# Optimization experiments

Hardware: AMD Instinct MI355X
Metric: run time of the kernel (lower is better)

Reference implementation:

```python
import jax, jax.numpy as jnp
import numpy as np

# graph layout constants
B = 64        # number of graphs
NPG = 512     # nodes per graph
N = B * NPG   # total nodes
DEG = 16      # avg degree
E = N * DEG   # total edges
F_IN = 256
H, C = 4, 64  # heads, per-head dim
K = NPG // 2  # topk pooling keeps ratio=0.5 per graph


def setup_inputs() -> dict:
    key = jax.random.key(0)
    ks = jax.random.split(key, 8)
    x = jax.random.normal(ks[0], (N, F_IN), dtype=jnp.float32)
    # within-graph random edges (src -> dst), contiguous node ids per graph
    offs = jnp.repeat(jnp.arange(B, dtype=jnp.int64) * NPG, NPG * DEG)
    src = offs + jax.random.randint(ks[1], (E,), 0, NPG)
    dst = offs + jax.random.randint(ks[2], (E,), 0, NPG)
    edge_index = jnp.stack([src, dst]).astype(jnp.int64)
    W = jax.random.normal(ks[3], (F_IN, H, C), dtype=jnp.float32) / np.sqrt(F_IN)
    att_src = jax.random.normal(ks[4], (H, C), dtype=jnp.float32) / np.sqrt(C)
    att_dst = jax.random.normal(ks[5], (H, C), dtype=jnp.float32) / np.sqrt(C)
    bias = jnp.zeros((H * C,), dtype=jnp.float32)
    bn_gamma = jnp.ones((H * C,), dtype=jnp.float32)
    bn_beta = jnp.zeros((H * C,), dtype=jnp.float32)
    pool_weight = jax.random.normal(ks[6], (H * C,), dtype=jnp.float32) / np.sqrt(H * C)
    return {"x": x, "edge_index": edge_index, "W": W, "att_src": att_src,
            "att_dst": att_dst, "bias": bias, "bn_gamma": bn_gamma,
            "bn_beta": bn_beta, "pool_weight": pool_weight}


def reference(x, edge_index, W, att_src, att_dst, bias, bn_gamma, bn_beta, pool_weight):
    n = x.shape[0]
    # --- GATConv ---
    h = jnp.einsum('nf,fhc->nhc', x, W)                 # [N,H,C]
    a_src = jnp.sum(h * att_src, axis=-1)               # [N,H]
    a_dst = jnp.sum(h * att_dst, axis=-1)               # [N,H]
    loops = jnp.arange(n, dtype=edge_index.dtype)        # add_self_loops=True default
    src = jnp.concatenate([edge_index[0], loops])
    dst = jnp.concatenate([edge_index[1], loops])
    e = jax.nn.leaky_relu(a_src[src] + a_dst[dst], 0.2)  # [E+N,H]
    # scatter-softmax over edges grouped by destination node
    emax = jax.ops.segment_max(e, dst, num_segments=n)
    ex = jnp.exp(e - emax[dst])
    den = jax.ops.segment_sum(ex, dst, num_segments=n)
    alpha = ex / (den[dst] + 1e-16)                      # [E+N,H]
    msg = alpha[:, :, None] * h[src]                     # [E+N,H,C]
    out = jax.ops.segment_sum(msg, dst, num_segments=n)  # [N,H,C]
    feat = out.reshape(n, H * C) + bias                  # concat heads
    # --- ReLU + BatchNorm (batch stats, training mode) ---
    feat = jax.nn.relu(feat)
    mean = jnp.mean(feat, axis=0)
    var = jnp.var(feat, axis=0)
    feat = (feat - mean) * jax.lax.rsqrt(var + 1e-5) * bn_gamma + bn_beta
    # --- TopKPooling (score = x.w/||w||, keep top ratio per graph, gate by tanh) ---
    score = feat @ pool_weight / jnp.linalg.norm(pool_weight)  # [N]
    top_s, top_i = jax.lax.top_k(score.reshape(B, NPG), K)     # [B,K]
    fg = feat.reshape(B, NPG, H * C)
    sel = jnp.take_along_axis(fg, top_i[:, :, None], axis=1)    # [B,K,HC]
    pooled = sel * jnp.tanh(top_s)[:, :, None]
    return pooled.reshape(B * K, H * C)
```

## Files before the change

### kernel.cpp

```cpp
#include <hip/hip_runtime.h>
#include <math.h>

#define N_NODES 32768
#define NPG 512
#define NGRAPH 64
#define KKEEP 256
#define CAP 64

typedef __attribute__((ext_vector_type(8))) short short8;
typedef __attribute__((ext_vector_type(4))) float f32x4;

__device__ __forceinline__ unsigned short f2bf(float v) {
  unsigned u = __builtin_bit_cast(unsigned, v);
  u = (u + 0x7FFFu + ((u >> 16) & 1u)) >> 16;
  return (unsigned short)u;
}
__device__ __forceinline__ float bf2f(unsigned short u) {
  unsigned v = ((unsigned)u) << 16;
  return __builtin_bit_cast(float, v);
}

__global__ __launch_bounds__(256) void k_hist_conv(
    const int* __restrict__ ei, int E, int* __restrict__ cnt,
    unsigned short* __restrict__ nbr,
    const float* __restrict__ x, const float* __restrict__ W,
    unsigned short* __restrict__ xh, unsigned short* __restrict__ xl,
    unsigned short* __restrict__ wth, unsigned short* __restrict__ wtl,
    unsigned short* __restrict__ wtll) {
  const int t = threadIdx.x;
  if (blockIdx.x < 2048) {
    int e = blockIdx.x * 256 + t;
    if (e < E) {
      int s = ei[e];
      int d = ei[E + e];
      int slot = atomicAdd(&cnt[d], 1);
      if (slot < CAP) nbr[(size_t)d * CAP + slot] = (unsigned short)(s & (NPG - 1));
    }
  } else if (blockIdx.x < 4096) {
    size_t base = ((size_t)(blockIdx.x - 2048) * 256 + t) * 16;
    unsigned short hb[16], lb[16];
#pragma unroll
    for (int g = 0; g < 4; g++) {
      float4 v = *(const float4*)&x[base + g * 4];
      float f[4] = {v.x, v.y, v.z, v.w};
#pragma unroll
      for (int j = 0; j < 4; j++) {
        unsigned short hh = f2bf(f[j]);
        float e1 = f[j] - bf2f(hh);
        hb[g * 4 + j] = hh;
        lb[g * 4 + j] = f2bf(e1);
      }
    }
    *(uint4*)&xh[base] = *(uint4*)&hb[0];
    *(uint4*)&xh[base + 8] = *(uint4*)&hb[8];
    *(uint4*)&xl[base] = *(uint4*)&lb[0];
    *(uint4*)&xl[base + 8] = *(uint4*)&lb[8];
  } else {
    int bw = blockIdx.x - 4096;
    int n = bw * 4 + (t >> 6);
    int k = (t & 63) * 4;
    unsigned short hb[4], lb[4], qb[4];
#pragma unroll
    for (int j = 0; j < 4; j++) {
      float v = W[(size_t)(k + j) * 256 + n];
      unsigned short hh = f2bf(v);
      float e1 = v - bf2f(hh);
      unsigned short ll = f2bf(e1);
      float e2 = e1 - bf2f(ll);
      hb[j] = hh; lb[j] = ll; qb[j] = f2bf(e2);
    }
    *(uint2*)&wth[(size_t)n * 256 + k] = *(uint2*)&hb[0];
    *(uint2*)&wtl[(size_t)n * 256 + k] = *(uint2*)&lb[0];
    *(uint2*)&wtll[(size_t)n * 256 + k] = *(uint2*)&qb[0];
  }
}

__global__ __launch_bounds__(256) void k_gemm(
    const float* __restrict__ x,
    const unsigned short* __restrict__ xhp, const unsigned short* __restrict__ xlp,
    const unsigned short* __restrict__ wth, const unsigned short* __restrict__ wtl,
    const unsigned short* __restrict__ wtll,
    const float* __restrict__ attS, const float* __restrict__ attD,
    float* __restrict__ h, float* __restrict__ a_src, float* __restrict__ a_dst) {
  __shared__ unsigned short As[3][128][40];
  __shared__ unsigned short Bs[3][128][40];
  const int t = threadIdx.x;
  const int mb = blockIdx.x >> 1, nh = blockIdx.x & 1;
  const int row0 = mb * 128;
  const int wid = t >> 6, lane = t & 63;
  const int q = lane >> 4, ln = lane & 15;
  const int wm = (wid >> 1) * 64, wn = (wid & 1) * 64;
  f32x4 acc[4][4] = {};

  for (int kc = 0; kc < 8; kc++) {
    const int k0 = kc * 32;
#pragma unroll
    for (int i = 0; i < 2; i++) {
      int c = i * 256 + t;
      int r = c >> 2, ko = (c & 3) * 8;
      size_t ga = (size_t)(row0 + r) * 256 + k0 + ko;
      uint4 vh = *(const uint4*)&xhp[ga];
      uint4 vl = *(const uint4*)&xlp[ga];
      *(uint4*)&As[0][r][ko] = vh;
      *(uint4*)&As[1][r][ko] = vl;
      float4 f0 = *(const float4*)&x[ga];
      float4 f1 = *(const float4*)&x[ga + 4];
      unsigned short hs[8], ls[8], qs[8];
      *(uint4*)&hs[0] = vh;
      *(uint4*)&ls[0] = vl;
      float ff[8] = {f0.x, f0.y, f0.z, f0.w, f1.x, f1.y, f1.z, f1.w};
#pragma unroll
      for (int j = 0; j < 8; j++)
        qs[j] = f2bf(ff[j] - bf2f(hs[j]) - bf2f(ls[j]));
      *(uint4*)&As[2][r][ko] = *(uint4*)&qs[0];
      size_t gb = (size_t)(nh * 128 + r) * 256 + k0 + ko;
      *(uint4*)&Bs[0][r][ko] = *(const uint4*)&wth[gb];
      *(uint4*)&Bs[1][r][ko] = *(const uint4*)&wtl[gb];
      *(uint4*)&Bs[2][r][ko] = *(const uint4*)&wtll[gb];
    }
    __syncthreads();
    short8 ah[4], al[4], aq[4];
#pragma unroll
    for (int mt = 0; mt < 4; mt++) {
      ah[mt] = *(const short8*)&As[0][wm + mt * 16 + ln][q * 8];
      al[mt] = *(const short8*)&As[1][wm + mt * 16 + ln][q * 8];
      aq[mt] = *(const short8*)&As[2][wm + mt * 16 + ln][q * 8];
    }
#pragma unroll
    for (int nt = 0; nt < 4; nt++) {
      short8 bh = *(const short8*)&Bs[0][wn + nt * 16 + ln][q * 8];
      short8 bl = *(const short8*)&Bs[1][wn + nt * 16 + ln][q * 8];
      short8 bq = *(const short8*)&Bs[2][wn + nt * 16 + ln][q * 8];
#pragma unroll
      for (int mt = 0; mt < 4; mt++) {
        acc[mt][nt] = __builtin_amdgcn_mfma_f32_16x16x32_bf16(ah[mt], bh, acc[mt][nt], 0, 0, 0);
        acc[mt][nt] = __builtin_amdgcn_mfma_f32_16x16x32_bf16(ah[mt], bl, acc[mt][nt], 0, 0, 0);
        acc[mt][nt] = __builtin_amdgcn_mfma_f32_16x16x32_bf16(al[mt], bh, acc[mt][nt], 0, 0, 0);
        acc[mt][nt] = __builtin_amdgcn_mfma_f32_16x16x32_bf16(ah[mt], bq, acc[mt][nt], 0, 0, 0);
        acc[mt][nt] = __builtin_amdgcn_mfma_f32_16x16x32_bf16(al[mt], bl, acc[mt][nt], 0, 0, 0);
        acc[mt][nt] = __builtin_amdgcn_mfma_f32_16x16x32_bf16(aq[mt], bh, acc[mt][nt], 0, 0, 0);
      }
    }
    __syncthreads();
  }
  const int head = nh * 2 + (wid & 1);
  float sA[4], sD[4];
#pragma unroll
  for (int nt = 0; nt < 4; nt++) {
    int n = nh * 128 + wn + nt * 16 + ln;
    sA[nt] = attS[n];
    sD[nt] = attD[n];
  }
#pragma unroll
  for (int mt = 0; mt < 4; mt++) {
#pragma unroll
    for (int reg = 0; reg < 4; reg++) {
      int m = row0 + wm + mt * 16 + q * 4 + reg;
      float ps = 0.f, pd = 0.f;
#pragma unroll
      for (int nt = 0; nt < 4; nt++) {
        float v = acc[mt][nt][reg];
        h[(size_t)m * 256 + nh * 128 + wn + nt * 16 + ln] = v;
        ps = fmaf(v, sA[nt], ps);
        pd = fmaf(v, sD[nt], pd);
      }
#pragma unroll
      for (int d = 1; d < 16; d <<= 1) {
        ps += __shfl_xor(ps, d, 16);
        pd += __shfl_xor(pd, d, 16);
      }
      if (ln == 0) {
        a_src[m * 4 + head] = ps;
        a_dst[m * 4 + head] = pd;
      }
    }
  }
}

__global__ __launch_bounds__(256) void k_agg(
    const float* __restrict__ h, const float* __restrict__ a_src,
    const float* __restrict__ a_dst, const int* __restrict__ cnt,
    const unsigned short* __restrict__ nbr, const float* __restrict__ bias,
    float* __restrict__ feat) {
  __shared__ float p_lds[4][68][4];
  __shared__ int s_lds[4][68];
  const int wv = threadIdx.x >> 6;
  const int lane = threadIdx.x & 63;
  int nb = (blockIdx.x & 7) * (N_NODES / 4 / 8) + (blockIdx.x >> 3);
  const int node = nb * 4 + wv;
  const int head = lane >> 4;
  const int li = lane & 15;
  const int c0 = lane * 4;
  const int base = node & ~(NPG - 1);
  const float ad = a_dst[node * 4 + head];
  int n = cnt[node];
  if (n > CAP) n = CAP;
  float e_reg[5];
  int srcs[5];
  int nit = 0;
  float m = -1e30f;
  for (int j = li; j <= n; j += 16) {
    int s = (j < n) ? base + (int)nbr[(size_t)node * CAP + j] : node;
    float e = a_src[s * 4 + head] + ad;
    e = (e > 0.f) ? e : 0.2f * e;
    srcs[nit] = s;
    e_reg[nit++] = e;
    m = fmaxf(m, e);
  }
#pragma unroll
  for (int d = 1; d < 16; d <<= 1) m = fmaxf(m, __shfl_xor(m, d, 16));
  float l = 0.f;
  for (int i = 0; i < nit; i++) {
    int j = li + i * 16;
    float p = __expf(e_reg[i] - m);
    l += p;
    p_lds[wv][j][head] = p;
    if (head == 0) s_lds[wv][j] = srcs[i];
  }
#pragma unroll
  for (int d = 1; d < 16; d <<= 1) l += __shfl_xor(l, d, 16);
  const float linv = 1.f / (l + 1e-16f);
  __builtin_amdgcn_s_waitcnt(0);
  float4 acc0 = make_float4(0.f, 0.f, 0.f, 0.f);
  float4 acc1 = make_float4(0.f, 0.f, 0.f, 0.f);
  int j = 0;
  for (; j + 1 <= n; j += 2) {
    float p0 = p_lds[wv][j][head];
    float p1 = p_lds[wv][j + 1][head];
    int s0 = s_lds[wv][j];
    int s1 = s_lds[wv][j + 1];
    float4 h0 = *(const float4*)&h[(size_t)s0 * 256 + c0];
    float4 h1 = *(const float4*)&h[(size_t)s1 * 256 + c0];
    acc0.x = fmaf(p0, h0.x, acc0.x); acc1.x = fmaf(p1, h1.x, acc1.x);
    acc0.y = fmaf(p0, h0.y, acc0.y); acc1.y = fmaf(p1, h1.y, acc1.y);
    acc0.z = fmaf(p0, h0.z, acc0.z); acc1.z = fmaf(p1, h1.z, acc1.z);
    acc0.w = fmaf(p0, h0.w, acc0.w); acc1.w = fmaf(p1, h1.w, acc1.w);
  }
  if (j <= n) {
    float p0 = p_lds[wv][j][head];
    int s0 = s_lds[wv][j];
    float4 h0 = *(const float4*)&h[(size_t)s0 * 256 + c0];
    acc0.x = fmaf(p0, h0.x, acc0.x);
    acc0.y = fmaf(p0, h0.y, acc0.y);
    acc0.z = fmaf(p0, h0.z, acc0.z);
    acc0.w = fmaf(p0, h0.w, acc0.w);
  }
  const float4 b4 = *(const float4*)&bias[c0];
  float4 o;
  o.x = fmaxf(fmaf(acc0.x + acc1.x, linv, b4.x), 0.f);
  o.y = fmaxf(fmaf(acc0.y + acc1.y, linv, b4.y), 0.f);
  o.z = fmaxf(fmaf(acc0.z + acc1.z, linv, b4.z), 0.f);
  o.w = fmaxf(fmaf(acc0.w + acc1.w, linv, b4.w), 0.f);
  *(float4*)&feat[(size_t)node * 256 + c0] = o;
}

__global__ __launch_bounds__(256) void k_bn_partial(const float* __restrict__ feat,
                                                    double* __restrict__ psum,
                                                    double* __restrict__ psq) {
  const int c = threadIdx.x;
  const int r0 = blockIdx.x * 128;
  double s = 0.0, q = 0.0;
  for (int i = 0; i < 128; i++) {
    double v = (double)feat[(size_t)(r0 + i) * 256 + c];
    s += v;
    q += v * v;
  }
  psum[blockIdx.x * 256 + c] = s;
  psq[blockIdx.x * 256 + c] = q;
}

__global__ __launch_bounds__(1024) void k_bn_final(
    const double* __restrict__ psum, const double* __restrict__ psq,
    const float* __restrict__ gam, const float* __restrict__ bet,
    const float* __restrict__ pw, float* __restrict__ cA, float* __restrict__ cB,
    float* __restrict__ sv) {
  __shared__ double reds[4][256];
  __shared__ double redq[4][256];
  __shared__ double wsq[256];
  __shared__ double sb[256];
  const int t = threadIdx.x;
  const int c = t & 255, sl = t >> 8;
  double s = 0.0, q = 0.0;
  for (int i = sl * 64; i < sl * 64 + 64; i++) {
    s += psum[i * 256 + c];
    q += psq[i * 256 + c];
  }
  reds[sl][c] = s;
  redq[sl][c] = q;
  if (sl == 0) {
    double w = (double)pw[c];
    wsq[c] = w * w;
  }
  __syncthreads();
  if (t == 0) {
    double nn = 0.0;
    for (int i = 0; i < 256; i++) nn += wsq[i];
    wsq[0] = sqrt(nn);
  }
  __syncthreads();
  if (sl == 0) {
    s = reds[0][c] + reds[1][c] + reds[2][c] + reds[3][c];
    q = redq[0][c] + redq[1][c] + redq[2][c] + redq[3][c];
    double mean = s / (double)N_NODES;
    double var = q / (double)N_NODES - mean * mean;
    double a = (double)gam[c] / sqrt(var + 1e-5);
    double cb = (double)bet[c] - mean * a;
    cA[c] = (float)a;
    cB[c] = (float)cb;
    double pwnv = (double)pw[c] / wsq[0];
    sv[c] = (float)(a * pwnv);
    sb[c] = cb * pwnv;
  }
  __syncthreads();
  if (t == 0) {
    double s0 = 0.0;
    for (int i = 0; i < 256; i++) s0 += sb[i];
    sv[256] = (float)s0;
  }
}

__global__ __launch_bounds__(256) void k_score(
    const float* __restrict__ feat, const float* __restrict__ sv,
    float* __restrict__ score) {
  const int lane = threadIdx.x & 63;
  const int node = blockIdx.x * 4 + (threadIdx.x >> 6);
  const int c0 = lane * 4;
  float4 f = *(const float4*)&feat[(size_t)node * 256 + c0];
  float4 w = *(const float4*)&sv[c0];
  float p = f.x * w.x + f.y * w.y + f.z * w.z + f.w * w.w;
#pragma unroll
  for (int d = 1; d < 64; d <<= 1) p += __shfl_xor(p, d, 64);
  if (lane == 0) score[node] = p + sv[256];
}

__global__ __launch_bounds__(256) void k_topk(
    const float* __restrict__ score, const float* __restrict__ feat,
    const float* __restrict__ cA, const float* __restrict__ cB,
    float* __restrict__ out) {
  __shared__ float ss[NPG];
  __shared__ int rnk[64];
  __shared__ float gt[64];
  const int g = blockIdx.x >> 3;
  const int part = blockIdx.x & 7;
  const int t = threadIdx.x;
  ss[t] = score[g * NPG + t];
  ss[t + 256] = score[g * NPG + t + 256];
  __syncthreads();
  const int ln = t & 3;
  const int ndl = part * 64 + (t >> 2);
  const float s = ss[ndl];
  int rank = 0;
  for (int j = ln * 128; j < ln * 128 + 128; j++) {
    float sj = ss[j];
    rank += (sj > s || (sj == s && j < ndl)) ? 1 : 0;
  }
  rank += __shfl_xor(rank, 1);
  rank += __shfl_xor(rank, 2);
  if (ln == 0) {
    rnk[t >> 2] = rank;
    gt[t >> 2] = tanhf(s);
  }
  __syncthreads();
  for (int idx = t; idx < 64 * 64; idx += 256) {
    int r = idx >> 6;
    int rank2 = rnk[r];
    if (rank2 < KKEEP) {
      int c4 = (idx & 63) * 4;
      int node = g * NPG + part * 64 + r;
      float4 f = *(const float4*)&feat[(size_t)node * 256 + c4];
      float4 a = *(const float4*)&cA[c4];
      float4 b = *(const float4*)&cB[c4];
      float tg = gt[r];
      float4 o;
      o.x = fmaf(f.x, a.x, b.x) * tg;
      o.y = fmaf(f.y, a.y, b.y) * tg;
      o.z = fmaf(f.z, a.z, b.z) * tg;
      o.w = fmaf(f.w, a.w, b.w) * tg;
      *(float4*)&out[(size_t)(g * KKEEP + rank2) * 256 + c4] = o;
    }
  }
}

extern "C" void kernel_launch(void* const* d_in, const int* in_sizes, int n_in,
                              void* d_out, int out_size, void* d_ws, size_t ws_size,
                              hipStream_t stream) {
  const float* x    = (const float*)d_in[0];
  const int*   ei   = (const int*)d_in[1];
  const float* W    = (const float*)d_in[2];
  const float* attS = (const float*)d_in[3];
  const float* attD = (const float*)d_in[4];
  const float* bias = (const float*)d_in[5];
  const float* gam  = (const float*)d_in[6];
  const float* bet  = (const float*)d_in[7];
  const float* pw   = (const float*)d_in[8];
  float* out = (float*)d_out;
  const int E = in_sizes[1] / 2;

  char* p = (char*)d_ws;
  float* h     = (float*)p; p += (size_t)N_NODES * 256 * 4;
  char* region = p;         p += (size_t)N_NODES * 256 * 4;
  unsigned short* xh = (unsigned short*)region;
  unsigned short* xl = (unsigned short*)(region + (size_t)N_NODES * 256 * 2);
  float* feat  = (float*)region;
  float* a_src = (float*)p; p += (size_t)N_NODES * 4 * 4;
  float* a_dst = (float*)p; p += (size_t)N_NODES * 4 * 4;
  float* score = (float*)p; p += (size_t)N_NODES * 4;
  double* psum = (double*)p; p += (size_t)256 * 256 * 8;
  double* psq  = (double*)p; p += (size_t)256 * 256 * 8;
  float* cA    = (float*)p; p += 256 * 4;
  float* cB    = (float*)p; p += 256 * 4;
  float* sv    = (float*)p; p += 260 * 4;
  unsigned short* wth  = (unsigned short*)p; p += (size_t)256 * 256 * 2;
  unsigned short* wtl  = (unsigned short*)p; p += (size_t)256 * 256 * 2;
  unsigned short* wtll = (unsigned short*)p; p += (size_t)256 * 256 * 2;
  int* cnt     = (int*)p;   p += (size_t)N_NODES * 4;
  unsigned short* nbr = (unsigned short*)p; p += (size_t)N_NODES * CAP * 2;

  hipMemsetAsync(cnt, 0, (size_t)N_NODES * 4, stream);
  k_hist_conv<<<4160, 256, 0, stream>>>(ei, E, cnt, nbr, x, W, xh, xl, wth, wtl, wtll);
  k_gemm<<<512, 256, 0, stream>>>(x, xh, xl, wth, wtl, wtll, attS, attD, h, a_src, a_dst);
  k_agg<<<N_NODES / 4, 256, 0, stream>>>(h, a_src, a_dst, cnt, nbr, bias, feat);
  k_bn_partial<<<256, 256, 0, stream>>>(feat, psum, psq);
  k_bn_final<<<1, 1024, 0, stream>>>(psum, psq, gam, bet, pw, cA, cB, sv);
  k_score<<<N_NODES / 4, 256, 0, stream>>>(feat, sv, score);
  k_topk<<<NGRAPH * 8, 256, 0, stream>>>(score, feat, cA, cB, out);
}
```

Before: 231.4 us.

## Restructure GEMM LDS layout, swizzle block order, and reduce attention dots via LDS

Result: faster. 222.1 us (-4.0%).

```diff
diff --git a/kernel.cpp b/kernel.cpp
--- a/kernel.cpp
+++ b/kernel.cpp
@@ -82,10 +82,11 @@
     const unsigned short* __restrict__ wtll,
     const float* __restrict__ attS, const float* __restrict__ attD,
     float* __restrict__ h, float* __restrict__ a_src, float* __restrict__ a_dst) {
-  __shared__ unsigned short As[3][128][40];
-  __shared__ unsigned short Bs[3][128][40];
+  __shared__ unsigned short lds[24576];
   const int t = threadIdx.x;
-  const int mb = blockIdx.x >> 1, nh = blockIdx.x & 1;
+  const int bid = blockIdx.x;
+  const int mb = (bid & 7) * 32 + (bid >> 4);
+  const int nh = (bid >> 3) & 1;
   const int row0 = mb * 128;
   const int wid = t >> 6, lane = t & 63;
   const int q = lane >> 4, ln = lane & 15;
@@ -97,12 +98,12 @@
 #pragma unroll
     for (int i = 0; i < 2; i++) {
       int c = i * 256 + t;
-      int r = c >> 2, ko = (c & 3) * 8;
-      size_t ga = (size_t)(row0 + r) * 256 + k0 + ko;
+      int r = c >> 2, cq = c & 3;
+      size_t ga = (size_t)(row0 + r) * 256 + k0 + cq * 8;
       uint4 vh = *(const uint4*)&xhp[ga];
       uint4 vl = *(const uint4*)&xlp[ga];
-      *(uint4*)&As[0][r][ko] = vh;
-      *(uint4*)&As[1][r][ko] = vl;
+      *(uint4*)&lds[((0 * 4 + cq) * 128 + r) * 8] = vh;
+      *(uint4*)&lds[((1 * 4 + cq) * 128 + r) * 8] = vl;
       float4 f0 = *(const float4*)&x[ga];
       float4 f1 = *(const float4*)&x[ga + 4];
       unsigned short hs[8], ls[8], qs[8];
@@ -112,25 +113,27 @@
 #pragma unroll
       for (int j = 0; j < 8; j++)
         qs[j] = f2bf(ff[j] - bf2f(hs[j]) - bf2f(ls[j]));
-      *(uint4*)&As[2][r][ko] = *(uint4*)&qs[0];
-      size_t gb = (size_t)(nh * 128 + r) * 256 + k0 + ko;
-      *(uint4*)&Bs[0][r][ko] = *(const uint4*)&wth[gb];
-      *(uint4*)&Bs[1][r][ko] = *(const uint4*)&wtl[gb];
-      *(uint4*)&Bs[2][r][ko] = *(const uint4*)&wtll[gb];
+      *(uint4*)&lds[((2 * 4 + cq) * 128 + r) * 8] = *(uint4*)&qs[0];
+      size_t gb = (size_t)(nh * 128 + r) * 256 + k0 + cq * 8;
+      *(uint4*)&lds[12288 + ((0 * 4 + cq) * 128 + r) * 8] = *(const uint4*)&wth[gb];
+      *(uint4*)&lds[12288 + ((1 * 4 + cq) * 128 + r) * 8] = *(const uint4*)&wtl[gb];
+      *(uint4*)&lds[12288 + ((2 * 4 + cq) * 128 + r) * 8] = *(const uint4*)&wtll[gb];
     }
     __syncthreads();
     short8 ah[4], al[4], aq[4];
 #pragma unroll
     for (int mt = 0; mt < 4; mt++) {
-      ah[mt] = *(const short8*)&As[0][wm + mt * 16 + ln][q * 8];
-      al[mt] = *(const short8*)&As[1][wm + mt * 16 + ln][q * 8];
-      aq[mt] = *(const short8*)&As[2][wm + mt * 16 + ln][q * 8];
+      int r = wm + mt * 16 + ln;
+      ah[mt] = *(const short8*)&lds[((0 * 4 + q) * 128 + r) * 8];
+      al[mt] = *(const short8*)&lds[((1 * 4 + q) * 128 + r) * 8];
+      aq[mt] = *(const short8*)&lds[((2 * 4 + q) * 128 + r) * 8];
     }
 #pragma unroll
     for (int nt = 0; nt < 4; nt++) {
-      short8 bh = *(const short8*)&Bs[0][wn + nt * 16 + ln][q * 8];
-      short8 bl = *(const short8*)&Bs[1][wn + nt * 16 + ln][q * 8];
-      short8 bq = *(const short8*)&Bs[2][wn + nt * 16 + ln][q * 8];
+      int r = wn + nt * 16 + ln;
+      short8 bh = *(const short8*)&lds[12288 + ((0 * 4 + q) * 128 + r) * 8];
+      short8 bl = *(const short8*)&lds[12288 + ((1 * 4 + q) * 128 + r) * 8];
+      short8 bq = *(const short8*)&lds[12288 + ((2 * 4 + q) * 128 + r) * 8];
 #pragma unroll
       for (int mt = 0; mt < 4; mt++) {
         acc[mt][nt] = __builtin_amdgcn_mfma_f32_16x16x32_bf16(ah[mt], bh, acc[mt][nt], 0, 0, 0);
@@ -151,6 +154,7 @@
     sA[nt] = attS[n];
     sD[nt] = attD[n];
   }
+  float2* epi = (float2*)lds;
 #pragma unroll
   for (int mt = 0; mt < 4; mt++) {
 #pragma unroll
@@ -164,16 +168,23 @@
         ps = fmaf(v, sA[nt], ps);
         pd = fmaf(v, sD[nt], pd);
       }
-#pragma unroll
-      for (int d = 1; d < 16; d <<= 1) {
-        ps += __shfl_xor(ps, d, 16);
-        pd += __shfl_xor(pd, d, 16);
-      }
-      if (ln == 0) {
-        a_src[m * 4 + head] = ps;
-        a_dst[m * 4 + head] = pd;
-      }
-    }
+      epi[(((wid * 4 + q) * 16) + mt * 4 + reg) * 18 + ln] = make_float2(ps, pd);
+    }
+  }
+  __syncthreads();
+  {
+    const int q2 = lane >> 4, rr = lane & 15;
+    const int base = (((wid * 4 + q2) * 16) + rr) * 18;
+    float ps = 0.f, pd = 0.f;
+#pragma unroll
+    for (int i = 0; i < 16; i++) {
+      float2 v = epi[base + i];
+      ps += v.x;
+      pd += v.y;
+    }
+    int m = row0 + wm + (rr >> 2) * 16 + q2 * 4 + (rr & 3);
+    a_src[m * 4 + head] = ps;
+    a_dst[m * 4 + head] = pd;
   }
 }
 
```
